# Performance work log

Measured on AMD Instinct MI355X. Metric: run time of the kernel, lower is better.

The kernel has to match this reference:

```python
import jax, jax.numpy as jnp
import numpy as np

DIM = 1024
HEADS = 16
HEAD_DIM = DIM // HEADS
EPS = 1e-5


def _layer_norm(z, g, b):
    m = jnp.mean(z, axis=-1, keepdims=True)
    v = jnp.var(z, axis=-1, keepdims=True)
    return (z - m) * jax.lax.rsqrt(v + EPS) * g + b


def setup_inputs() -> dict:
    key = jax.random.key(0)
    ks = jax.random.split(key, 8)
    B, T, S = 2, 2048, 2048
    x = jax.random.normal(ks[0], (B, T, DIM), dtype=jnp.float32)
    context = jax.random.normal(ks[1], (B, S, DIM), dtype=jnp.float32)
    w_qkv = jax.random.normal(ks[2], (DIM, 3 * DIM), dtype=jnp.float32) * 0.02
    b_qkv = jnp.zeros((3 * DIM,), dtype=jnp.float32)
    w_out = jax.random.normal(ks[3], (DIM, DIM), dtype=jnp.float32) * 0.02
    b_out = jnp.zeros((DIM,), dtype=jnp.float32)
    ln_g = jnp.ones((DIM,), dtype=jnp.float32)
    ln_b = jnp.zeros((DIM,), dtype=jnp.float32)
    return {"x": x, "context": context, "w_qkv": w_qkv, "b_qkv": b_qkv,
            "w_out": w_out, "b_out": b_out, "ln_g": ln_g, "ln_b": ln_b}


def reference(x, context, w_qkv, b_qkv, w_out, b_out, ln_g, ln_b):
    B, T, C = x.shape
    S = context.shape[1]
    scale = HEAD_DIM ** -0.5

    def split_heads(z):  # [B, L, C] -> [B, H, L, Dh]
        return z.reshape(z.shape[0], z.shape[1], HEADS, HEAD_DIM).transpose(0, 2, 1, 3)

    # self qkv
    qkv = _layer_norm(x, ln_g, ln_b) @ w_qkv + b_qkv  # [B, T, 3C]
    q = split_heads(qkv[..., :C])
    k = split_heads(qkv[..., C:2 * C])
    v = split_heads(qkv[..., 2 * C:])

    # context k, v from the shared qkv projection (K/V slices)
    ckv = _layer_norm(context, ln_g, ln_b) @ w_qkv + b_qkv  # [B, S, 3C]
    ck = split_heads(ckv[..., C:2 * C])
    cv = split_heads(ckv[..., 2 * C:])

    k = jnp.concatenate([k, ck], axis=2)  # [B, H, T+S, Dh]
    v = jnp.concatenate([v, cv], axis=2)

    attn = jax.nn.softmax(jnp.einsum('bhtd,bhsd->bhts', q, k) * scale, axis=-1)
    out = jnp.einsum('bhts,bhsd->bhtd', attn, v)  # [B, H, T, Dh]
    out = out.transpose(0, 2, 1, 3).reshape(B, T, C)
    return out @ w_out + b_out + x
```

## Files before the change

kernel.cpp:

```cpp
#include <hip/hip_runtime.h>
#include <stdint.h>

#define H 16
#define DH 64
#define T 2048
#define SS 2048
#define L 4096
#define DIM 1024
#define BB 2

typedef __bf16 bf16x8 __attribute__((ext_vector_type(8)));
typedef float f32x4 __attribute__((ext_vector_type(4)));
typedef float f32x16 __attribute__((ext_vector_type(16)));
typedef unsigned u32x4 __attribute__((ext_vector_type(4)));

__device__ __forceinline__ unsigned short f2bf(float f){
  unsigned u = __builtin_bit_cast(unsigned, f);
  u += 0x7fff + ((u >> 16) & 1);
  return (unsigned short)(u >> 16);
}

__device__ __forceinline__ unsigned cvt_pk_bf16(float lo, float hi){
  unsigned r;
  asm("v_cvt_pk_bf16_f32 %0, %1, %2" : "=v"(r) : "v"(lo), "v"(hi));
  return r;
}

__device__ __forceinline__ void gload_lds16(const void* g, void* l){
  void* gnc = const_cast<void*>(g);
  __builtin_amdgcn_global_load_lds((__attribute__((address_space(1))) void*)gnc,
                                   (__attribute__((address_space(3))) void*)l, 16, 0, 0);
}

__global__ __launch_bounds__(256) void ln_kernel(const float* __restrict__ x, const float* __restrict__ ctx,
                          const float* __restrict__ g, const float* __restrict__ b,
                          unsigned short* __restrict__ out){
  int row = blockIdx.x;
  int tid = threadIdx.x;
  const float* src = (row < BB*T) ? (x + (size_t)row*DIM) : (ctx + (size_t)(row - BB*T)*DIM);
  float4 v = reinterpret_cast<const float4*>(src)[tid];
  float s  = v.x + v.y + v.z + v.w;
  float s2 = v.x*v.x + v.y*v.y + v.z*v.z + v.w*v.w;
  #pragma unroll
  for (int off = 32; off > 0; off >>= 1){
    s  += __shfl_down(s,  off, 64);
    s2 += __shfl_down(s2, off, 64);
  }
  __shared__ float red[8];
  if ((tid & 63) == 0){ red[(tid>>6)*2] = s; red[(tid>>6)*2+1] = s2; }
  __syncthreads();
  s  = red[0] + red[2] + red[4] + red[6];
  s2 = red[1] + red[3] + red[5] + red[7];
  float mean = s * (1.0f/DIM);
  float var  = s2 * (1.0f/DIM) - mean*mean;
  float rstd = rsqrtf(var + 1e-5f);
  float4 gg = reinterpret_cast<const float4*>(g)[tid];
  float4 bv = reinterpret_cast<const float4*>(b)[tid];
  ushort4 o;
  o.x = f2bf((v.x-mean)*rstd*gg.x + bv.x);
  o.y = f2bf((v.y-mean)*rstd*gg.y + bv.y);
  o.z = f2bf((v.z-mean)*rstd*gg.z + bv.z);
  o.w = f2bf((v.w-mean)*rstd*gg.w + bv.w);
  reinterpret_cast<ushort4*>(out + (size_t)row*DIM)[tid] = o;
}

__global__ __launch_bounds__(256) void transpose_f32_bf16(const float* __restrict__ in,
                          unsigned short* __restrict__ out, int R, int C){
  __shared__ float tile[32][33];
  int c0 = blockIdx.x*32, r0 = blockIdx.y*32;
  int tx = threadIdx.x, ty = threadIdx.y;
  #pragma unroll
  for (int k = 0; k < 4; k++)
    tile[ty + k*8][tx] = in[(size_t)(r0 + ty + k*8)*C + c0 + tx];
  __syncthreads();
  #pragma unroll
  for (int k = 0; k < 4; k++)
    out[(size_t)(c0 + ty + k*8)*R + r0 + tx] = f2bf(tile[tx][ty + k*8]);
}

__global__ __launch_bounds__(256) void qkv_gemm(const unsigned short* __restrict__ A,
      const unsigned short* __restrict__ Bt, const float* __restrict__ bias,
      unsigned short* __restrict__ qbuf, unsigned short* __restrict__ kbuf,
      unsigned short* __restrict__ vtbuf){
  int n0 = blockIdx.x*128, m0 = blockIdx.y*128;
  if (m0 >= BB*T && n0 < DIM) return;
  __shared__ unsigned short at[128*32];
  __shared__ unsigned short btile[128*32];
  int tid = threadIdx.x, lane = tid & 63, wv = tid >> 6;
  int wm = (wv >> 1)*64, wn = (wv & 1)*64;
  f32x4 acc[4][4];
  #pragma unroll
  for (int i = 0; i < 4; i++)
    #pragma unroll
    for (int j = 0; j < 4; j++) acc[i][j] = (f32x4){0.f,0.f,0.f,0.f};

  for (int k0 = 0; k0 < DIM; k0 += 32){
    #pragma unroll
    for (int c = 0; c < 2; c++){
      int idx = c*256 + tid;
      int row = idx >> 2, koff = (idx & 3)*16;
      gload_lds16((const char*)A  + ((size_t)(m0+row)*DIM + k0)*2 + koff,
                  (char*)at + (c*256 + wv*64)*16);
      gload_lds16((const char*)Bt + ((size_t)(n0+row)*DIM + k0)*2 + koff,
                  (char*)btile + (c*256 + wv*64)*16);
    }
    __syncthreads();
    bf16x8 af[4], bfv[4];
    #pragma unroll
    for (int i = 0; i < 4; i++){
      af[i]  = *reinterpret_cast<const bf16x8*>((const char*)at    + (wm + i*16 + (lane&15))*64 + (lane>>4)*16);
      bfv[i] = *reinterpret_cast<const bf16x8*>((const char*)btile + (wn + i*16 + (lane&15))*64 + (lane>>4)*16);
    }
    #pragma unroll
    for (int mi = 0; mi < 4; mi++)
      #pragma unroll
      for (int ni = 0; ni < 4; ni++)
        acc[mi][ni] = __builtin_amdgcn_mfma_f32_16x16x32_bf16(af[mi], bfv[ni], acc[mi][ni], 0,0,0);
    __syncthreads();
  }

  #pragma unroll
  for (int ni = 0; ni < 4; ni++){
    int gn = n0 + wn + ni*16 + (lane & 15);
    float bv = bias[gn];
    int sec = gn >> 10, cc = gn & 1023, hh = cc >> 6, d = cc & 63;
    #pragma unroll
    for (int mi = 0; mi < 4; mi++){
      int gmb = m0 + wm + mi*16 + ((lane >> 4) << 2);
      bool isctx = gmb >= BB*T;
      int rm = isctx ? gmb - BB*T : gmb;
      int bidx = rm >> 11, tt = rm & 2047;
      size_t bh = (size_t)bidx*H + hh;
      if (sec == 0){
        if (isctx) continue;
        #pragma unroll
        for (int r = 0; r < 4; r++)
          qbuf[(bh*T + tt + r)*DH + d] = f2bf((acc[mi][ni][r] + bv)*0.18033688f);
      } else if (sec == 1){
        int j = isctx ? T + tt : tt;
        #pragma unroll
        for (int r = 0; r < 4; r++)
          kbuf[(bh*L + j + r)*DH + d] = f2bf(acc[mi][ni][r] + bv);
      } else {
        int j = isctx ? T + tt : tt;
        ushort4 o;
        o.x = f2bf(acc[mi][ni][0] + bv);
        o.y = f2bf(acc[mi][ni][1] + bv);
        o.z = f2bf(acc[mi][ni][2] + bv);
        o.w = f2bf(acc[mi][ni][3] + bv);
        *reinterpret_cast<ushort4*>(vtbuf + (bh*DH + d)*L + j) = o;
      }
    }
  }
}

__global__ __launch_bounds__(256) void attn_kernel(const unsigned short* __restrict__ q,
      const unsigned short* __restrict__ kbuf, const unsigned short* __restrict__ vtbuf,
      unsigned short* __restrict__ ao){
  int hw = blockIdx.x;
  int wid = (hw & 7)*64 + (hw >> 3);
  int qt = wid & 15, hb = wid >> 4;
  int hh = hb & 15, b = hb >> 4;
  int tid = threadIdx.x, lane = tid & 63, wv = tid >> 6;
  int hi = lane >> 5, q32 = lane & 31;
  __shared__ unsigned short kt[2][64*64];
  __shared__ unsigned short vtt[2][64*64];
  size_t bh = (size_t)b*H + hh;
  int qbase = qt*128 + wv*32;

  const unsigned short* qp = q + (bh*T + qbase + q32)*DH + hi*8;
  bf16x8 qf[4];
  #pragma unroll
  for (int ks = 0; ks < 4; ks++)
    qf[ks] = *reinterpret_cast<const bf16x8*>(qp + ks*16);

  f32x16 o_acc[2];
  #pragma unroll
  for (int d = 0; d < 2; d++)
    #pragma unroll
    for (int i = 0; i < 16; i++) o_acc[d][i] = 0.f;
  float m_l = -1e30f, l_acc = 0.f;

  const char* kg = (const char*)(kbuf + bh*(size_t)L*DH);
  const char* vg = (const char*)(vtbuf + bh*(size_t)DH*L);

  #define STAGE(bufi, jt) { \
    _Pragma("unroll") \
    for (int c = 0; c < 2; c++){ \
      int idx = c*256 + tid; \
      int row = idx >> 3, c16 = idx & 7; \
      int sc16 = c16 ^ (row & 7); \
      gload_lds16(kg + (size_t)(jt)*8192 + row*128 + sc16*16, \
                  (char*)kt[bufi] + (c*256 + wv*64)*16); \
      gload_lds16(vg + (size_t)row*(L*2) + (jt)*128 + sc16*16, \
                  (char*)vtt[bufi] + (c*256 + wv*64)*16); \
    } }

  STAGE(0, 0);
  __syncthreads();

  for (int jt = 0; jt < L/64; ++jt){
    int bufi = jt & 1;
    if (jt + 1 < L/64) STAGE(bufi^1, jt+1);
    const char* kb = (const char*)kt[bufi];
    const char* vb = (const char*)vtt[bufi];

    f32x16 sc[2];
    #pragma unroll
    for (int t = 0; t < 2; t++)
      #pragma unroll
      for (int i = 0; i < 16; i++) sc[t][i] = 0.f;
    #pragma unroll
    for (int ks = 0; ks < 4; ks++){
      #pragma unroll
      for (int t = 0; t < 2; t++){
        int row = t*32 + q32;
        bf16x8 kf = *reinterpret_cast<const bf16x8*>(kb + row*128 + (((ks*2+hi) ^ (row&7))*16));
        sc[t] = __builtin_amdgcn_mfma_f32_32x32x16_bf16(kf, qf[ks], sc[t], 0,0,0);
      }
    }

    float tm = sc[0][0];
    #pragma unroll
    for (int t = 0; t < 2; t++)
      #pragma unroll
      for (int i = 0; i < 16; i++) tm = fmaxf(tm, sc[t][i]);
    if (!__all(tm - m_l <= 8.0f)){
      float tmf = fmaxf(tm, __shfl_xor(tm, 32, 64));
      float mn = fmaxf(m_l, tmf);
      float alpha = exp2f(m_l - mn);
      m_l = mn;
      #pragma unroll
      for (int d = 0; d < 2; d++)
        #pragma unroll
        for (int i = 0; i < 16; i++) o_acc[d][i] *= alpha;
      l_acc *= alpha;
    }
    #pragma unroll
    for (int t = 0; t < 2; t++)
      #pragma unroll
      for (int i = 0; i < 16; i++){
        float p = exp2f(sc[t][i] - m_l);
        sc[t][i] = p; l_acc += p;
      }

    bf16x8 pfrag[4];
    #pragma unroll
    for (int t = 0; t < 2; t++){
      #pragma unroll
      for (int half = 0; half < 2; half++){
        unsigned p01 = cvt_pk_bf16(sc[t][half*8+0], sc[t][half*8+1]);
        unsigned p23 = cvt_pk_bf16(sc[t][half*8+2], sc[t][half*8+3]);
        unsigned p45 = cvt_pk_bf16(sc[t][half*8+4], sc[t][half*8+5]);
        unsigned p67 = cvt_pk_bf16(sc[t][half*8+6], sc[t][half*8+7]);
        asm("v_permlane32_swap_b32 %0, %1" : "+v"(p01), "+v"(p45));
        asm("v_permlane32_swap_b32 %0, %1" : "+v"(p23), "+v"(p67));
        u32x4 w = (u32x4){p01, p23, p45, p67};
        pfrag[t*2 + half] = __builtin_bit_cast(bf16x8, w);
      }
    }

    #pragma unroll
    for (int ks = 0; ks < 4; ks++){
      #pragma unroll
      for (int d = 0; d < 2; d++){
        int row = d*32 + q32;
        bf16x8 vf = *reinterpret_cast<const bf16x8*>(vb + row*128 + (((ks*2+hi) ^ (row&7))*16));
        o_acc[d] = __builtin_amdgcn_mfma_f32_32x32x16_bf16(vf, pfrag[ks], o_acc[d], 0,0,0);
      }
    }
    __syncthreads();
  }

  float l_tot = l_acc + __shfl_xor(l_acc, 32, 64);
  float inv = 1.0f / l_tot;
  unsigned short* aop = ao + ((size_t)b*T + qbase + q32)*DIM + hh*DH;
  #pragma unroll
  for (int d = 0; d < 2; d++)
    #pragma unroll
    for (int rg = 0; rg < 4; rg++){
      int d0 = d*32 + rg*8 + hi*4;
      ushort4 o;
      o.x = __builtin_bit_cast(unsigned short, (__bf16)(o_acc[d][rg*4+0]*inv));
      o.y = __builtin_bit_cast(unsigned short, (__bf16)(o_acc[d][rg*4+1]*inv));
      o.z = __builtin_bit_cast(unsigned short, (__bf16)(o_acc[d][rg*4+2]*inv));
      o.w = __builtin_bit_cast(unsigned short, (__bf16)(o_acc[d][rg*4+3]*inv));
      *reinterpret_cast<ushort4*>(aop + d0) = o;
    }
}

__global__ __launch_bounds__(256) void out_gemm(const unsigned short* __restrict__ A,
      const unsigned short* __restrict__ Bt, const float* __restrict__ bout,
      const float* __restrict__ xres, float* __restrict__ out){
  int n0 = blockIdx.x*128, m0 = blockIdx.y*128;
  __shared__ unsigned short at[128*32];
  __shared__ unsigned short btile[128*32];
  int tid = threadIdx.x, lane = tid & 63, wv = tid >> 6;
  int wm = (wv >> 1)*64, wn = (wv & 1)*64;
  f32x4 acc[4][4];
  #pragma unroll
  for (int i = 0; i < 4; i++)
    #pragma unroll
    for (int j = 0; j < 4; j++) acc[i][j] = (f32x4){0.f,0.f,0.f,0.f};

  for (int k0 = 0; k0 < DIM; k0 += 32){
    #pragma unroll
    for (int c = 0; c < 2; c++){
      int idx = c*256 + tid;
      int row = idx >> 2, koff = (idx & 3)*16;
      gload_lds16((const char*)A  + ((size_t)(m0+row)*DIM + k0)*2 + koff,
                  (char*)at + (c*256 + wv*64)*16);
      gload_lds16((const char*)Bt + ((size_t)(n0+row)*DIM + k0)*2 + koff,
                  (char*)btile + (c*256 + wv*64)*16);
    }
    __syncthreads();
    bf16x8 af[4], bfv[4];
    #pragma unroll
    for (int i = 0; i < 4; i++){
      af[i]  = *reinterpret_cast<const bf16x8*>((const char*)at    + (wm + i*16 + (lane&15))*64 + (lane>>4)*16);
      bfv[i] = *reinterpret_cast<const bf16x8*>((const char*)btile + (wn + i*16 + (lane&15))*64 + (lane>>4)*16);
    }
    #pragma unroll
    for (int mi = 0; mi < 4; mi++)
      #pragma unroll
      for (int ni = 0; ni < 4; ni++)
        acc[mi][ni] = __builtin_amdgcn_mfma_f32_16x16x32_bf16(af[mi], bfv[ni], acc[mi][ni], 0,0,0);
    __syncthreads();
  }

  #pragma unroll
  for (int ni = 0; ni < 4; ni++){
    int gn = n0 + wn + ni*16 + (lane & 15);
    float bv = bout[gn];
    #pragma unroll
    for (int mi = 0; mi < 4; mi++){
      int gmb = m0 + wm + mi*16 + ((lane >> 4) << 2);
      #pragma unroll
      for (int r = 0; r < 4; r++){
        int gm = gmb + r;
        out[(size_t)gm*DIM + gn] = acc[mi][ni][r] + bv + xres[(size_t)gm*DIM + gn];
      }
    }
  }
}

extern "C" void kernel_launch(void* const* d_in, const int* in_sizes, int n_in,
                              void* d_out, int out_size, void* d_ws, size_t ws_size,
                              hipStream_t stream){
  const float* x    = (const float*)d_in[0];
  const float* ctx  = (const float*)d_in[1];
  const float* wqkv = (const float*)d_in[2];
  const float* bqkv = (const float*)d_in[3];
  const float* wout = (const float*)d_in[4];
  const float* bout = (const float*)d_in[5];
  const float* lng  = (const float*)d_in[6];
  const float* lnb  = (const float*)d_in[7];
  float* out = (float*)d_out;

  char* ws = (char*)d_ws;
  unsigned short* wqkvT  = (unsigned short*)ws; ws += (size_t)3072*1024*2;
  unsigned short* woutT  = (unsigned short*)ws; ws += (size_t)1024*1024*2;
  unsigned short* ln_all = (unsigned short*)ws; ws += (size_t)8192*1024*2;
  unsigned short* qbuf   = (unsigned short*)ws; ws += (size_t)BB*H*T*DH*2;
  unsigned short* kbuf   = (unsigned short*)ws; ws += (size_t)BB*H*L*DH*2;
  unsigned short* vtbuf  = (unsigned short*)ws; ws += (size_t)BB*H*DH*L*2;
  unsigned short* aobuf  = (unsigned short*)ws; ws += (size_t)BB*T*DIM*2;

  transpose_f32_bf16<<<dim3(3072/32, 1024/32), dim3(32,8), 0, stream>>>(wqkv, wqkvT, 1024, 3072);
  transpose_f32_bf16<<<dim3(1024/32, 1024/32), dim3(32,8), 0, stream>>>(wout, woutT, 1024, 1024);
  ln_kernel<<<dim3(8192), dim3(256), 0, stream>>>(x, ctx, lng, lnb, ln_all);
  qkv_gemm<<<dim3(3072/128, 8192/128), dim3(256), 0, stream>>>(ln_all, wqkvT, bqkv, qbuf, kbuf, vtbuf);
  attn_kernel<<<dim3(512), dim3(256), 0, stream>>>(qbuf, kbuf, vtbuf, aobuf);
  out_gemm<<<dim3(1024/128, 4096/128), dim3(256), 0, stream>>>(aobuf, woutT, bout, x, out);
}
```

Baseline: 258.6 us.

## Widen attention KV tile to 128, sum softmax via MFMA, remap QKV grid

The attention kernel now processes 128 keys per iteration instead of 64, doubling the LDS buffers and halving the loop trip count and barriers. The row max uses v_max3, and the softmax denominator is accumulated by an extra MFMA against a ones vector instead of scalar adds and a final shuffle. Separately, the QKV GEMM gets a 1D grid with an XCD-style block remap to improve L2 locality. The risks are higher register and LDS pressure in the attention kernel, which could lower occupancy, plus extra MFMA work for the row sums.

```diff
diff --git a/kernel.cpp b/kernel.cpp
--- a/kernel.cpp
+++ b/kernel.cpp
@@ -23,6 +23,12 @@
 __device__ __forceinline__ unsigned cvt_pk_bf16(float lo, float hi){
   unsigned r;
   asm("v_cvt_pk_bf16_f32 %0, %1, %2" : "=v"(r) : "v"(lo), "v"(hi));
+  return r;
+}
+
+__device__ __forceinline__ float fmax3(float a, float b, float c){
+  float r;
+  asm("v_max3_f32 %0, %1, %2, %3" : "=v"(r) : "v"(a), "v"(b), "v"(c));
   return r;
 }
 
@@ -82,7 +88,9 @@
       const unsigned short* __restrict__ Bt, const float* __restrict__ bias,
       unsigned short* __restrict__ qbuf, unsigned short* __restrict__ kbuf,
       unsigned short* __restrict__ vtbuf){
-  int n0 = blockIdx.x*128, m0 = blockIdx.y*128;
+  int orig = blockIdx.x;
+  int wid = (orig & 7)*192 + (orig >> 3);
+  int n0 = (wid % 24)*128, m0 = (wid / 24)*128;
   if (m0 >= BB*T && n0 < DIM) return;
   __shared__ unsigned short at[128*32];
   __shared__ unsigned short btile[128*32];
@@ -163,8 +171,8 @@
   int hh = hb & 15, b = hb >> 4;
   int tid = threadIdx.x, lane = tid & 63, wv = tid >> 6;
   int hi = lane >> 5, q32 = lane & 31;
-  __shared__ unsigned short kt[2][64*64];
-  __shared__ unsigned short vtt[2][64*64];
+  __shared__ unsigned short kt[2][128*64];
+  __shared__ unsigned short vtt[2][64*128];
   size_t bh = (size_t)b*H + hh;
   int qbase = qt*128 + wv*32;
 
@@ -174,57 +182,70 @@
   for (int ks = 0; ks < 4; ks++)
     qf[ks] = *reinterpret_cast<const bf16x8*>(qp + ks*16);
 
-  f32x16 o_acc[2];
+  bf16x8 ones;
+  #pragma unroll
+  for (int j = 0; j < 8; j++) ones[j] = (__bf16)1.0f;
+
+  f32x16 o_acc[2], l_vec;
   #pragma unroll
   for (int d = 0; d < 2; d++)
     #pragma unroll
     for (int i = 0; i < 16; i++) o_acc[d][i] = 0.f;
-  float m_l = -1e30f, l_acc = 0.f;
+  #pragma unroll
+  for (int i = 0; i < 16; i++) l_vec[i] = 0.f;
+  float m_l = -1e30f;
 
   const char* kg = (const char*)(kbuf + bh*(size_t)L*DH);
   const char* vg = (const char*)(vtbuf + bh*(size_t)DH*L);
 
   #define STAGE(bufi, jt) { \
     _Pragma("unroll") \
-    for (int c = 0; c < 2; c++){ \
+    for (int c = 0; c < 4; c++){ \
       int idx = c*256 + tid; \
-      int row = idx >> 3, c16 = idx & 7; \
-      int sc16 = c16 ^ (row & 7); \
-      gload_lds16(kg + (size_t)(jt)*8192 + row*128 + sc16*16, \
+      int krow = idx >> 3, kc = idx & 7; \
+      gload_lds16(kg + (size_t)((jt)*128 + krow)*128 + ((kc ^ (krow & 7))*16), \
                   (char*)kt[bufi] + (c*256 + wv*64)*16); \
-      gload_lds16(vg + (size_t)row*(L*2) + (jt)*128 + sc16*16, \
+      int vrow = idx >> 4, vc = idx & 15; \
+      gload_lds16(vg + (size_t)vrow*(L*2) + (jt)*256 + ((vc ^ (vrow & 7))*16), \
                   (char*)vtt[bufi] + (c*256 + wv*64)*16); \
     } }
 
   STAGE(0, 0);
   __syncthreads();
 
-  for (int jt = 0; jt < L/64; ++jt){
+  for (int jt = 0; jt < L/128; ++jt){
     int bufi = jt & 1;
-    if (jt + 1 < L/64) STAGE(bufi^1, jt+1);
+    if (jt + 1 < L/128) STAGE(bufi^1, jt+1);
     const char* kb = (const char*)kt[bufi];
     const char* vb = (const char*)vtt[bufi];
 
-    f32x16 sc[2];
-    #pragma unroll
-    for (int t = 0; t < 2; t++)
+    f32x16 sc[4];
+    #pragma unroll
+    for (int t = 0; t < 4; t++)
       #pragma unroll
       for (int i = 0; i < 16; i++) sc[t][i] = 0.f;
     #pragma unroll
     for (int ks = 0; ks < 4; ks++){
       #pragma unroll
-      for (int t = 0; t < 2; t++){
+      for (int t = 0; t < 4; t++){
         int row = t*32 + q32;
         bf16x8 kf = *reinterpret_cast<const bf16x8*>(kb + row*128 + (((ks*2+hi) ^ (row&7))*16));
         sc[t] = __builtin_amdgcn_mfma_f32_32x32x16_bf16(kf, qf[ks], sc[t], 0,0,0);
       }
     }
 
-    float tm = sc[0][0];
-    #pragma unroll
-    for (int t = 0; t < 2; t++)
-      #pragma unroll
-      for (int i = 0; i < 16; i++) tm = fmaxf(tm, sc[t][i]);
+    float rt[4];
+    #pragma unroll
+    for (int t = 0; t < 4; t++){
+      float v0 = fmax3(sc[t][0],  sc[t][1],  sc[t][2]);
+      float v1 = fmax3(sc[t][3],  sc[t][4],  sc[t][5]);
+      float v2 = fmax3(sc[t][6],  sc[t][7],  sc[t][8]);
+      float v3 = fmax3(sc[t][9],  sc[t][10], sc[t][11]);
+      float v4 = fmax3(sc[t][12], sc[t][13], sc[t][14]);
+      rt[t] = fmaxf(fmax3(v0, v1, v2), fmax3(v3, v4, sc[t][15]));
+    }
+    float tm = fmaxf(fmax3(rt[0], rt[1], rt[2]), rt[3]);
+
     if (!__all(tm - m_l <= 8.0f)){
       float tmf = fmaxf(tm, __shfl_xor(tm, 32, 64));
       float mn = fmaxf(m_l, tmf);
@@ -234,19 +255,17 @@
       for (int d = 0; d < 2; d++)
         #pragma unroll
         for (int i = 0; i < 16; i++) o_acc[d][i] *= alpha;
-      l_acc *= alpha;
-    }
-    #pragma unroll
-    for (int t = 0; t < 2; t++)
-      #pragma unroll
-      for (int i = 0; i < 16; i++){
-        float p = exp2f(sc[t][i] - m_l);
-        sc[t][i] = p; l_acc += p;
-      }
-
-    bf16x8 pfrag[4];
-    #pragma unroll
-    for (int t = 0; t < 2; t++){
+      l_vec[0] *= alpha;
+    }
+    #pragma unroll
+    for (int t = 0; t < 4; t++)
+      #pragma unroll
+      for (int i = 0; i < 16; i++)
+        sc[t][i] = exp2f(sc[t][i] - m_l);
+
+    bf16x8 pfrag[8];
+    #pragma unroll
+    for (int t = 0; t < 4; t++){
       #pragma unroll
       for (int half = 0; half < 2; half++){
         unsigned p01 = cvt_pk_bf16(sc[t][half*8+0], sc[t][half*8+1]);
@@ -261,19 +280,19 @@
     }
 
     #pragma unroll
-    for (int ks = 0; ks < 4; ks++){
+    for (int ks = 0; ks < 8; ks++){
       #pragma unroll
       for (int d = 0; d < 2; d++){
         int row = d*32 + q32;
-        bf16x8 vf = *reinterpret_cast<const bf16x8*>(vb + row*128 + (((ks*2+hi) ^ (row&7))*16));
+        bf16x8 vf = *reinterpret_cast<const bf16x8*>(vb + row*256 + (((ks*2+hi) ^ (row&7))*16));
         o_acc[d] = __builtin_amdgcn_mfma_f32_32x32x16_bf16(vf, pfrag[ks], o_acc[d], 0,0,0);
       }
-    }
-    __syncthreads();
-  }
-
-  float l_tot = l_acc + __shfl_xor(l_acc, 32, 64);
-  float inv = 1.0f / l_tot;
+      l_vec = __builtin_amdgcn_mfma_f32_32x32x16_bf16(ones, pfrag[ks], l_vec, 0,0,0);
+    }
+    __syncthreads();
+  }
+
+  float inv = 1.0f / l_vec[0];
   unsigned short* aop = ao + ((size_t)b*T + qbase + q32)*DIM + hh*DH;
   #pragma unroll
   for (int d = 0; d < 2; d++)
@@ -369,7 +388,7 @@
   transpose_f32_bf16<<<dim3(3072/32, 1024/32), dim3(32,8), 0, stream>>>(wqkv, wqkvT, 1024, 3072);
   transpose_f32_bf16<<<dim3(1024/32, 1024/32), dim3(32,8), 0, stream>>>(wout, woutT, 1024, 1024);
   ln_kernel<<<dim3(8192), dim3(256), 0, stream>>>(x, ctx, lng, lnb, ln_all);
-  qkv_gemm<<<dim3(3072/128, 8192/128), dim3(256), 0, stream>>>(ln_all, wqkvT, bqkv, qbuf, kbuf, vtbuf);
+  qkv_gemm<<<dim3(1536), dim3(256), 0, stream>>>(ln_all, wqkvT, bqkv, qbuf, kbuf, vtbuf);
   attn_kernel<<<dim3(512), dim3(256), 0, stream>>>(qbuf, kbuf, vtbuf, aobuf);
   out_gemm<<<dim3(1024/128, 4096/128), dim3(256), 0, stream>>>(aobuf, woutT, bout, x, out);
 }
```

New measurement: 250.6 us. 1.03x faster.
